# Kernel tuning notes

Hardware: AMD Instinct MI355X
Metric: run time of the kernel (lower is better)

Reference implementation:

```python
import jax, jax.numpy as jnp
import numpy as np

NLEVELS = 16
FEATURES = 2
TABLE_SIZE = 2 ** 18
MINRES, MAXRES = 16, 512
_b = (MAXRES / MINRES) ** (1.0 / (NLEVELS - 1))
RES = [int(np.floor(MINRES * _b ** l + 1e-6)) for l in range(NLEVELS)]
# Instant-NGP spatial hash primes (first prime is 1)
PRIMES = np.array([1, 2654435761, 805459861], dtype=np.uint32)


def _interp(coords, res, gather):
    """Trilinear interpolation. coords: [N,3] in [-1,1]; gather: [N,3]int -> [N,F]."""
    pos = jnp.clip((coords + 1.0) * 0.5 * (res - 1), 0.0, res - 1)  # [N,3] grid coords
    i0 = jnp.floor(pos)
    w = pos - i0                              # [N,3] fractional weights
    i0 = i0.astype(jnp.int32)
    out = jnp.zeros((coords.shape[0], FEATURES), coords.dtype)
    for corner in range(8):                   # 8 trilinear corners
        off = jnp.array([(corner >> 2) & 1, (corner >> 1) & 1, corner & 1], jnp.int32)
        idx = jnp.minimum(i0 + off, res - 1)  # clamp at boundary ('nearest' padding)
        wgt = jnp.prod(jnp.where(off == 1, w, 1.0 - w), axis=-1)  # [N]
        out = out + gather(idx) * wgt[:, None]
    return out  # [N, F]


def setup_inputs() -> dict:
    key = jax.random.key(0)
    k1, k2, k3 = jax.random.split(key, 3)
    N = 2 ** 21
    coords = jax.random.uniform(k1, (N, 3), jnp.float32, -1.0, 1.0)
    dense_grid = jax.random.uniform(k2, (FEATURES, RES[0], RES[0], RES[0]), jnp.float32, -1e-4, 1e-4)
    hash_tables = jax.random.uniform(k3, (NLEVELS - 1, FEATURES, TABLE_SIZE), jnp.float32, -1e-4, 1e-4)
    return {"coords": coords, "dense_grid": dense_grid, "hash_tables": hash_tables}


def reference(coords, dense_grid, hash_tables):
    feats = []
    R0 = RES[0]
    gflat = dense_grid.reshape(FEATURES, -1)  # [F, R0^3]

    def dense_gather(idx):
        flat = (idx[:, 0] * R0 + idx[:, 1]) * R0 + idx[:, 2]
        return gflat[:, flat].T               # [N, F]

    feats.append(_interp(coords, R0, dense_gather))

    primes = jnp.asarray(PRIMES)
    for l in range(1, NLEVELS):
        table = hash_tables[l - 1]            # [F, T]

        def hash_gather(idx, table=table):
            u = idx.astype(jnp.uint32) * primes
            h = (u[:, 0] ^ u[:, 1] ^ u[:, 2]) % TABLE_SIZE
            return table[:, h].T              # [N, F]

        feats.append(_interp(coords, RES[l], hash_gather))

    return jnp.concatenate(feats, axis=-1)    # [N, NLEVELS*FEATURES]
```

## Files before the change

### kernel.cpp

```cpp
#include <hip/hip_runtime.h>

#define TS 262144
#define TMASK (TS - 1)
#define P2 2654435761u
#define P3 805459861u

__device__ __constant__ int c_res[16] = {16, 20, 25, 32, 40, 50, 64, 80,
                                         101, 128, 161, 203, 256, 322, 406, 512};

__global__ __launch_bounds__(256) void xpose_kernel(
    const float* __restrict__ dense, const float* __restrict__ tables,
    float2* __restrict__ ws) {
  int i = blockIdx.x * 256 + threadIdx.x;
  const int total = 15 * TS;
  if (i < total) {
    int l = i >> 18;
    int h = i & TMASK;
    const float* t = tables + (size_t)l * (2 * TS);
    ws[4096 + i] = make_float2(t[h], t[TS + h]);
  } else {
    int j = i - total;
    if (j < 4096) ws[j] = make_float2(dense[j], dense[4096 + j]);
  }
}

template <bool XP>
__global__ __launch_bounds__(256) void encode_kernel(
    const float* __restrict__ coords,
    const float* __restrict__ dense,
    const float* __restrict__ tables,
    const float2* __restrict__ xtab,
    float2* __restrict__ out, int npts) {
  __shared__ float s_c[48];
  __shared__ int s_res[16];
  const int tid = threadIdx.x;
  const int lvl = tid & 15;
  const int pin = tid >> 4;
  const int pbase = blockIdx.x * 16;

  if (tid < 48) {
    int gi = pbase * 3 + tid;
    s_c[tid] = (gi < npts * 3) ? coords[gi] : 0.0f;
  }
  if (tid < 16) s_res[tid] = c_res[tid];
  __syncthreads();

  const int n = pbase + pin;
  if (n >= npts) return;

  const float cx = s_c[pin * 3 + 0];
  const float cy = s_c[pin * 3 + 1];
  const float cz = s_c[pin * 3 + 2];
  const int res = s_res[lvl];
  const int r1 = res - 1;
  const float rm1 = (float)r1;

  float px = fminf(fmaxf((cx + 1.0f) * 0.5f * rm1, 0.0f), rm1);
  float py = fminf(fmaxf((cy + 1.0f) * 0.5f * rm1, 0.0f), rm1);
  float pz = fminf(fmaxf((cz + 1.0f) * 0.5f * rm1, 0.0f), rm1);
  float fx = floorf(px), fy = floorf(py), fz = floorf(pz);
  float wx = px - fx, wy = py - fy, wz = pz - fz;
  int ix0 = (int)fx, iy0 = (int)fy, iz0 = (int)fz;
  int ix1 = min(ix0 + 1, r1), iy1 = min(iy0 + 1, r1), iz1 = min(iz0 + 1, r1);

  const bool dl = (lvl == 0);
  unsigned hx0, hx1, hy0, hy1, hz0, hz1;
  if (dl) {
    hx0 = (unsigned)ix0 << 8; hx1 = (unsigned)ix1 << 8;
    hy0 = (unsigned)iy0 << 4; hy1 = (unsigned)iy1 << 4;
    hz0 = (unsigned)iz0;      hz1 = (unsigned)iz1;
  } else {
    hx0 = (unsigned)ix0;      hx1 = (unsigned)ix1;
    hy0 = (unsigned)iy0 * P2; hy1 = (unsigned)iy1 * P2;
    hz0 = (unsigned)iz0 * P3; hz1 = (unsigned)iz1 * P3;
  }

  unsigned idx[8];
  float wgt[8];
#pragma unroll
  for (int c = 0; c < 8; ++c) {
    unsigned hx = (c & 4) ? hx1 : hx0;
    unsigned hy = (c & 2) ? hy1 : hy0;
    unsigned hz = (c & 1) ? hz1 : hz0;
    idx[c] = (hx ^ hy ^ hz) & TMASK;
    float a = (c & 4) ? wx : 1.0f - wx;
    float b = (c & 2) ? wy : 1.0f - wy;
    float d = (c & 1) ? wz : 1.0f - wz;
    wgt[c] = a * b * d;
  }

  float acc0 = 0.0f, acc1 = 0.0f;
  if (XP) {
    const float2* tab = xtab + (dl ? 0 : (4096 + (size_t)(lvl - 1) * TS));
    float2 v[8];
#pragma unroll
    for (int c = 0; c < 8; ++c) v[c] = tab[idx[c]];
#pragma unroll
    for (int c = 0; c < 8; ++c) {
      acc0 = fmaf(v[c].x, wgt[c], acc0);
      acc1 = fmaf(v[c].y, wgt[c], acc1);
    }
  } else {
    const float* t0;
    unsigned fs;
    if (dl) { t0 = dense; fs = 4096; }
    else    { t0 = tables + (size_t)(lvl - 1) * (2 * TS); fs = TS; }
    float v0[8], v1[8];
#pragma unroll
    for (int c = 0; c < 8; ++c) { v0[c] = t0[idx[c]]; v1[c] = t0[fs + idx[c]]; }
#pragma unroll
    for (int c = 0; c < 8; ++c) {
      acc0 = fmaf(v0[c], wgt[c], acc0);
      acc1 = fmaf(v1[c], wgt[c], acc1);
    }
  }

  out[(size_t)n * 16 + lvl] = make_float2(acc0, acc1);
}

extern "C" void kernel_launch(void* const* d_in, const int* in_sizes, int n_in,
                              void* d_out, int out_size, void* d_ws, size_t ws_size,
                              hipStream_t stream) {
  const float* coords = (const float*)d_in[0];
  const float* dense  = (const float*)d_in[1];
  const float* tables = (const float*)d_in[2];
  float2* out = (float2*)d_out;
  const int npts = in_sizes[0] / 3;
  const int eblocks = (npts + 15) / 16;
  const size_t need = (size_t)(4096 + 15 * TS) * sizeof(float2);

  if (ws_size >= need) {
    float2* ws = (float2*)d_ws;
    const int tblocks = (15 * TS + 4096 + 255) / 256;
    hipLaunchKernelGGL(xpose_kernel, dim3(tblocks), dim3(256), 0, stream,
                       dense, tables, ws);
    hipLaunchKernelGGL((encode_kernel<true>), dim3(eblocks), dim3(256), 0, stream,
                       coords, dense, tables, ws, out, npts);
  } else {
    hipLaunchKernelGGL((encode_kernel<false>), dim3(eblocks), dim3(256), 0, stream,
                       coords, dense, tables, (const float2*)nullptr, out, npts);
  }
}
```

Baseline: 1.864 ms.

## Map one thread per point looping all levels, with block-wide level sync

Changes the work split so that each thread handles one point and loops over all 16 levels, instead of one thread per (point, level) pair. A __syncthreads after each level keeps the block's threads on the same level table, which is meant to keep each table's working set hot in cache. Output is written as eight float4 stores per point, and coords are staged through shared memory with nontemporal loads. The risks are 16x fewer threads, more registers for the 32 accumulators, and per-level barriers that may lower occupancy and latency hiding for the random gathers.

```diff
diff --git a/kernel.cpp b/kernel.cpp
--- a/kernel.cpp
+++ b/kernel.cpp
@@ -4,9 +4,6 @@
 #define TMASK (TS - 1)
 #define P2 2654435761u
 #define P3 805459861u
-
-__device__ __constant__ int c_res[16] = {16, 20, 25, 32, 40, 50, 64, 80,
-                                         101, 128, 161, 203, 256, 322, 406, 512};
 
 __global__ __launch_bounds__(256) void xpose_kernel(
     const float* __restrict__ dense, const float* __restrict__ tables,
@@ -30,92 +27,102 @@
     const float* __restrict__ dense,
     const float* __restrict__ tables,
     const float2* __restrict__ xtab,
-    float2* __restrict__ out, int npts) {
-  __shared__ float s_c[48];
-  __shared__ int s_res[16];
+    float4* __restrict__ out, int npts) {
+  constexpr int RESA[16] = {16, 20, 25, 32, 40, 50, 64, 80,
+                            101, 128, 161, 203, 256, 322, 406, 512};
+  __shared__ float s_c[768];
   const int tid = threadIdx.x;
-  const int lvl = tid & 15;
-  const int pin = tid >> 4;
-  const int pbase = blockIdx.x * 16;
+  const int pbase = blockIdx.x * 256;
 
-  if (tid < 48) {
-    int gi = pbase * 3 + tid;
-    s_c[tid] = (gi < npts * 3) ? coords[gi] : 0.0f;
+#pragma unroll
+  for (int j = 0; j < 3; ++j) {
+    int gi = pbase * 3 + j * 256 + tid;
+    s_c[j * 256 + tid] = (gi < npts * 3) ? __builtin_nontemporal_load(&coords[gi]) : 0.0f;
   }
-  if (tid < 16) s_res[tid] = c_res[tid];
   __syncthreads();
 
-  const int n = pbase + pin;
-  if (n >= npts) return;
+  const int n = pbase + tid;
+  const bool valid = n < npts;
+  const float cxn = (s_c[tid * 3 + 0] + 1.0f) * 0.5f;
+  const float cyn = (s_c[tid * 3 + 1] + 1.0f) * 0.5f;
+  const float czn = (s_c[tid * 3 + 2] + 1.0f) * 0.5f;
 
-  const float cx = s_c[pin * 3 + 0];
-  const float cy = s_c[pin * 3 + 1];
-  const float cz = s_c[pin * 3 + 2];
-  const int res = s_res[lvl];
-  const int r1 = res - 1;
-  const float rm1 = (float)r1;
+  float acc[32];
 
-  float px = fminf(fmaxf((cx + 1.0f) * 0.5f * rm1, 0.0f), rm1);
-  float py = fminf(fmaxf((cy + 1.0f) * 0.5f * rm1, 0.0f), rm1);
-  float pz = fminf(fmaxf((cz + 1.0f) * 0.5f * rm1, 0.0f), rm1);
-  float fx = floorf(px), fy = floorf(py), fz = floorf(pz);
-  float wx = px - fx, wy = py - fy, wz = pz - fz;
-  int ix0 = (int)fx, iy0 = (int)fy, iz0 = (int)fz;
-  int ix1 = min(ix0 + 1, r1), iy1 = min(iy0 + 1, r1), iz1 = min(iz0 + 1, r1);
+#pragma unroll
+  for (int lvl = 0; lvl < 16; ++lvl) {
+    const int res = RESA[lvl];
+    const int r1 = res - 1;
+    const float rm1 = (float)r1;
 
-  const bool dl = (lvl == 0);
-  unsigned hx0, hx1, hy0, hy1, hz0, hz1;
-  if (dl) {
-    hx0 = (unsigned)ix0 << 8; hx1 = (unsigned)ix1 << 8;
-    hy0 = (unsigned)iy0 << 4; hy1 = (unsigned)iy1 << 4;
-    hz0 = (unsigned)iz0;      hz1 = (unsigned)iz1;
-  } else {
-    hx0 = (unsigned)ix0;      hx1 = (unsigned)ix1;
-    hy0 = (unsigned)iy0 * P2; hy1 = (unsigned)iy1 * P2;
-    hz0 = (unsigned)iz0 * P3; hz1 = (unsigned)iz1 * P3;
+    float px = fminf(fmaxf(cxn * rm1, 0.0f), rm1);
+    float py = fminf(fmaxf(cyn * rm1, 0.0f), rm1);
+    float pz = fminf(fmaxf(czn * rm1, 0.0f), rm1);
+    float fx = floorf(px), fy = floorf(py), fz = floorf(pz);
+    float wx = px - fx, wy = py - fy, wz = pz - fz;
+    int ix0 = (int)fx, iy0 = (int)fy, iz0 = (int)fz;
+    int ix1 = min(ix0 + 1, r1), iy1 = min(iy0 + 1, r1), iz1 = min(iz0 + 1, r1);
+
+    unsigned hx0, hx1, hy0, hy1, hz0, hz1;
+    if (lvl == 0) {
+      hx0 = (unsigned)ix0 << 8; hx1 = (unsigned)ix1 << 8;
+      hy0 = (unsigned)iy0 << 4; hy1 = (unsigned)iy1 << 4;
+      hz0 = (unsigned)iz0;      hz1 = (unsigned)iz1;
+    } else {
+      hx0 = (unsigned)ix0;      hx1 = (unsigned)ix1;
+      hy0 = (unsigned)iy0 * P2; hy1 = (unsigned)iy1 * P2;
+      hz0 = (unsigned)iz0 * P3; hz1 = (unsigned)iz1 * P3;
+    }
+
+    unsigned idx[8];
+    float wgt[8];
+#pragma unroll
+    for (int c = 0; c < 8; ++c) {
+      unsigned hx = (c & 4) ? hx1 : hx0;
+      unsigned hy = (c & 2) ? hy1 : hy0;
+      unsigned hz = (c & 1) ? hz1 : hz0;
+      idx[c] = (hx ^ hy ^ hz) & TMASK;
+      float a = (c & 4) ? wx : 1.0f - wx;
+      float b = (c & 2) ? wy : 1.0f - wy;
+      float d = (c & 1) ? wz : 1.0f - wz;
+      wgt[c] = a * b * d;
+    }
+
+    float a0 = 0.0f, a1 = 0.0f;
+    if (XP) {
+      const float2* tab = (lvl == 0) ? xtab : (xtab + 4096 + (size_t)(lvl - 1) * TS);
+      float2 v[8];
+#pragma unroll
+      for (int c = 0; c < 8; ++c) v[c] = tab[idx[c]];
+#pragma unroll
+      for (int c = 0; c < 8; ++c) {
+        a0 = fmaf(v[c].x, wgt[c], a0);
+        a1 = fmaf(v[c].y, wgt[c], a1);
+      }
+    } else {
+      const float* t0 = (lvl == 0) ? dense : (tables + (size_t)(lvl - 1) * (2 * TS));
+      const unsigned fs = (lvl == 0) ? 4096u : (unsigned)TS;
+      float v0[8], v1[8];
+#pragma unroll
+      for (int c = 0; c < 8; ++c) { v0[c] = t0[idx[c]]; v1[c] = t0[fs + idx[c]]; }
+#pragma unroll
+      for (int c = 0; c < 8; ++c) {
+        a0 = fmaf(v0[c], wgt[c], a0);
+        a1 = fmaf(v1[c], wgt[c], a1);
+      }
+    }
+    acc[2 * lvl + 0] = a0;
+    acc[2 * lvl + 1] = a1;
+
+    __syncthreads();
   }
 
-  unsigned idx[8];
-  float wgt[8];
+  if (valid) {
+    float4* o = out + (size_t)n * 8;
 #pragma unroll
-  for (int c = 0; c < 8; ++c) {
-    unsigned hx = (c & 4) ? hx1 : hx0;
-    unsigned hy = (c & 2) ? hy1 : hy0;
-    unsigned hz = (c & 1) ? hz1 : hz0;
-    idx[c] = (hx ^ hy ^ hz) & TMASK;
-    float a = (c & 4) ? wx : 1.0f - wx;
-    float b = (c & 2) ? wy : 1.0f - wy;
-    float d = (c & 1) ? wz : 1.0f - wz;
-    wgt[c] = a * b * d;
+    for (int j = 0; j < 8; ++j)
+      o[j] = make_float4(acc[4 * j + 0], acc[4 * j + 1], acc[4 * j + 2], acc[4 * j + 3]);
   }
-
-  float acc0 = 0.0f, acc1 = 0.0f;
-  if (XP) {
-    const float2* tab = xtab + (dl ? 0 : (4096 + (size_t)(lvl - 1) * TS));
-    float2 v[8];
-#pragma unroll
-    for (int c = 0; c < 8; ++c) v[c] = tab[idx[c]];
-#pragma unroll
-    for (int c = 0; c < 8; ++c) {
-      acc0 = fmaf(v[c].x, wgt[c], acc0);
-      acc1 = fmaf(v[c].y, wgt[c], acc1);
-    }
-  } else {
-    const float* t0;
-    unsigned fs;
-    if (dl) { t0 = dense; fs = 4096; }
-    else    { t0 = tables + (size_t)(lvl - 1) * (2 * TS); fs = TS; }
-    float v0[8], v1[8];
-#pragma unroll
-    for (int c = 0; c < 8; ++c) { v0[c] = t0[idx[c]]; v1[c] = t0[fs + idx[c]]; }
-#pragma unroll
-    for (int c = 0; c < 8; ++c) {
-      acc0 = fmaf(v0[c], wgt[c], acc0);
-      acc1 = fmaf(v1[c], wgt[c], acc1);
-    }
-  }
-
-  out[(size_t)n * 16 + lvl] = make_float2(acc0, acc1);
 }
 
 extern "C" void kernel_launch(void* const* d_in, const int* in_sizes, int n_in,
@@ -124,9 +131,9 @@
   const float* coords = (const float*)d_in[0];
   const float* dense  = (const float*)d_in[1];
   const float* tables = (const float*)d_in[2];
-  float2* out = (float2*)d_out;
+  float4* out = (float4*)d_out;
   const int npts = in_sizes[0] / 3;
-  const int eblocks = (npts + 15) / 16;
+  const int eblocks = (npts + 255) / 256;
   const size_t need = (size_t)(4096 + 15 * TS) * sizeof(float2);
 
   if (ws_size >= need) {
```

New measurement: 1.497 ms. 1.24x faster.
